# Kernel optimization log

Measured on AMD Instinct MI355X. Metric: run time of the kernel, lower is better.

The kernel has to match this reference:

```python
import jax, jax.numpy as jnp
import numpy as np

EPS = 1e-06


def setup_inputs() -> dict:
    key = jax.random.key(0)
    ks = jax.random.split(key, 8)
    B, N, D, r, T, O, Hid = 32, 2048, 64, 32, 31, 12, 128
    in_dim = r + T  # 63
    xav = lambda k, shape: jax.random.uniform(k, shape, jnp.float32, -1.0, 1.0) * np.sqrt(6.0 / (shape[0] + shape[1]))
    return {
        "H": jax.random.normal(ks[0], (B, N, D), jnp.float32),
        "ts_out": jax.random.uniform(ks[1], (B, O, T), jnp.float32),
        "O": O,
        "P_raw": xav(ks[2], (N, r)),
        "Q_raw": xav(ks[3], (N, r)),
        "W1": xav(ks[4], (in_dim, Hid)),
        "b1": jnp.zeros((Hid,), jnp.float32),
        "W2": xav(ks[5], (Hid, r)),
        "b2": jnp.zeros((r,), jnp.float32),
        "alpha": jax.random.uniform(ks[6], (1,), jnp.float32),
    }


def reference(H, ts_out, O, P_raw, Q_raw, W1, b1, W2, b2, alpha):
    # nonnegative_basis=True -> softplus on both bases
    P = jax.nn.softplus(P_raw)  # [N, r]
    Q = jax.nn.softplus(Q_raw)  # [N, r]
    # Right contraction: U = Q^T H per batch -> [B, r, D]
    U = jnp.einsum('bnd,nr->brd', H, Q)
    # Context norm over feature dim: [B, r]
    ctx = jnp.sqrt(jnp.mean(U * U, axis=-1) + EPS)
    # Gate features: concat([ts_out [B,O,T], ctx broadcast to [B,O,r]])
    B = H.shape[0]
    ctx_exp = jnp.broadcast_to(ctx[:, None, :], (B, O, ctx.shape[-1]))
    feat = jnp.concatenate([ts_out, ctx_exp], axis=-1)  # [B, O, T+r]
    # scale MLP with exact (erf) GELU, dropout=0 (eval)
    h = jax.nn.gelu(feat @ W1 + b1, approximate=False)
    s = jax.nn.softplus(h @ W2 + b2)  # [B, O, r]
    # M = P (s \odot U) without materializing NxN: [B, O, N, D]
    M = jnp.einsum('bor,brd,nr->bond', s, U, P)
    a = jnp.clip(alpha[0], 0.0, 1.0)
    H_base = H[:, None, :, :]  # broadcast over O
    H_graph = H_base + a * (M - H_base)
    return H_graph
```

## Files before the change

### kernel.cpp

```cpp
#include <hip/hip_runtime.h>
#include <math.h>

#define B_ 32
#define N_ 2048
#define D_ 64
#define R_ 32
#define T_ 31
#define O_ 12
#define HID_ 128
#define IN_DIM_ 63
#define NCH_ 32

#define OFF_QSP   0
#define OFF_UPART (OFF_QSP + N_*R_)
#define OFF_U     (OFF_UPART + B_*NCH_*R_*D_)
#define OFF_CTX   (OFF_U + B_*R_*D_)
#define OFF_PBF   (OFF_CTX + B_*R_)
#define OFF_SUT   (OFF_PBF + N_*R_/2)

typedef __attribute__((ext_vector_type(4))) float f32x4;
typedef __attribute__((ext_vector_type(8))) short short8;

__device__ __forceinline__ float softplus_f(float x) {
    return fmaxf(x, 0.0f) + log1pf(expf(-fabsf(x)));
}
__device__ __forceinline__ float gelu_f(float x) {
    return 0.5f * x * (1.0f + erff(x * 0.70710678118654752440f));
}
__device__ __forceinline__ unsigned short f2bf(float f) {
    unsigned int u = __float_as_uint(f);
    u = (u + 0x7FFFu + ((u >> 16) & 1u)) >> 16;
    return (unsigned short)u;
}

__global__ __launch_bounds__(256) void k_softplus(const float* __restrict__ Qr,
                                                  const float* __restrict__ Pr,
                                                  float* __restrict__ ws) {
    int i = blockIdx.x * blockDim.x + threadIdx.x;
    if (i < N_ * R_) {
        ws[OFF_QSP + i] = softplus_f(Qr[i]);
    } else if (i < 2 * N_ * R_) {
        int j = i - N_ * R_;
        ((unsigned short*)(ws + OFF_PBF))[j] = f2bf(softplus_f(Pr[j]));
    }
}

__global__ __launch_bounds__(512) void k_upart(const float* __restrict__ H,
                                               float* __restrict__ ws) {
    const float* __restrict__ Qsp = ws + OFF_QSP;
    float* __restrict__ Upart = ws + OFF_UPART;
    int b = blockIdx.x / NCH_;
    int c = blockIdx.x % NCH_;
    int tid = threadIdx.x;
    int d = tid & 63;
    int rb = __builtin_amdgcn_readfirstlane(tid >> 6);
    const int r0 = rb * 4;
    float acc0 = 0.f, acc1 = 0.f, acc2 = 0.f, acc3 = 0.f;
    const int n0 = c * (N_ / NCH_);
    const float* __restrict__ Hb = H + (size_t)b * N_ * D_ + d;
    #pragma unroll 2
    for (int i = 0; i < N_ / NCH_; ++i) {
        int n = n0 + i;
        float h = Hb[(size_t)n * D_];
        const float* q = Qsp + (size_t)n * R_ + r0;
        acc0 = fmaf(h, q[0], acc0);
        acc1 = fmaf(h, q[1], acc1);
        acc2 = fmaf(h, q[2], acc2);
        acc3 = fmaf(h, q[3], acc3);
    }
    float* up = Upart + ((size_t)(b * NCH_ + c) * R_ + r0) * D_ + d;
    up[0 * D_] = acc0;
    up[1 * D_] = acc1;
    up[2 * D_] = acc2;
    up[3 * D_] = acc3;
}

__global__ __launch_bounds__(256) void k_ured(float* __restrict__ ws) {
    const float* __restrict__ Upart = ws + OFF_UPART;
    float* __restrict__ U = ws + OFF_U;
    float* __restrict__ ctx = ws + OFF_CTX;
    int b = blockIdx.x;
    int r = blockIdx.y * 4 + (threadIdx.x >> 6);
    int d = threadIdx.x & 63;
    float u = 0.f;
    #pragma unroll 8
    for (int c = 0; c < NCH_; ++c)
        u += Upart[((size_t)(b * NCH_ + c) * R_ + r) * D_ + d];
    U[((size_t)b * R_ + r) * D_ + d] = u;
    float sq = u * u;
    #pragma unroll
    for (int off = 32; off; off >>= 1) sq += __shfl_xor(sq, off, 64);
    if (d == 0) ctx[b * R_ + r] = sqrtf(sq * (1.0f / D_) + 1e-6f);
}

__global__ __launch_bounds__(128) void k_mlp(const float* __restrict__ ts_out,
                                             const float* __restrict__ W1,
                                             const float* __restrict__ b1,
                                             const float* __restrict__ W2,
                                             const float* __restrict__ b2,
                                             const float* __restrict__ alpha,
                                             float* __restrict__ ws) {
    __shared__ float feat[IN_DIM_];
    __shared__ float hsh[HID_];
    __shared__ float ssh[R_];
    int bo = blockIdx.x;
    int b = bo / O_;
    int tid = threadIdx.x;
    const float* __restrict__ ctx = ws + OFF_CTX;
    if (tid < T_) feat[tid] = ts_out[(size_t)bo * T_ + tid];
    else if (tid < IN_DIM_) feat[tid] = ctx[b * R_ + (tid - T_)];
    __syncthreads();
    float acc = b1[tid];
    #pragma unroll 9
    for (int k = 0; k < IN_DIM_; ++k) acc = fmaf(feat[k], W1[k * HID_ + tid], acc);
    hsh[tid] = gelu_f(acc);
    __syncthreads();
    if (tid < R_) {
        float a2 = b2[tid];
        #pragma unroll 8
        for (int j = 0; j < HID_; ++j) a2 = fmaf(hsh[j], W2[j * R_ + tid], a2);
        ssh[tid] = softplus_f(a2);
    }
    __syncthreads();
    float a = fminf(fmaxf(alpha[0], 0.0f), 1.0f);
    const float* __restrict__ U = ws + OFF_U;
    unsigned short* SUT = (unsigned short*)(ws + OFF_SUT) + (size_t)bo * D_ * R_;
    #pragma unroll
    for (int idx = tid; idx < D_ * R_; idx += 128) {
        int d = idx >> 5, r = idx & 31;
        SUT[idx] = f2bf(a * ssh[r] * U[((size_t)b * R_ + r) * D_ + d]);
    }
}

__global__ __launch_bounds__(256) void k_main(const float* __restrict__ H,
                                              const float* __restrict__ alpha,
                                              const float* __restrict__ ws,
                                              float* __restrict__ out) {
    __shared__ float tile[64 * 64];
    const int b = blockIdx.y;
    const int nblk = blockIdx.x * 64;
    const int tid = threadIdx.x;
    const int w = tid >> 6;
    const int lane = tid & 63;
    const int l16 = lane & 15;
    const int lhi = lane >> 4;
    const int rl = w * 16 + l16;
    const float a = fminf(fmaxf(alpha[0], 0.0f), 1.0f);
    const float oma = 1.0f - a;

    const unsigned short* Pbf = (const unsigned short*)(ws + OFF_PBF);
    const unsigned short* SUT0 = (const unsigned short*)(ws + OFF_SUT);

    short8 pfrag = *(const short8*)(Pbf + (size_t)(nblk + rl) * R_ + lhi * 8);

    const float* __restrict__ Hrow = H + ((size_t)b * N_ + nblk + rl) * D_;
    f32x4 homa[4];
    #pragma unroll
    for (int db = 0; db < 4; ++db)
        homa[db] = oma * *(const f32x4*)(Hrow + db * 16 + lhi * 4);

    char* tbytes = (char*)tile;
    float* __restrict__ oblk = out + ((size_t)(b * O_) * N_ + nblk) * D_;

    for (int o = 0; o < O_; ++o) {
        const unsigned short* SUT = SUT0 + (size_t)(b * O_ + o) * D_ * R_;
        #pragma unroll
        for (int db = 0; db < 4; ++db) {
            short8 sfrag = *(const short8*)(SUT + (size_t)(db * 16 + l16) * R_ + lhi * 8);
            f32x4 v = homa[db] + __builtin_amdgcn_mfma_f32_16x16x32_bf16(
                sfrag, pfrag, (f32x4){0.f, 0.f, 0.f, 0.f}, 0, 0, 0);
            int c = (db * 64 + lhi * 16) ^ ((rl & 7) << 4);
            *(f32x4*)(tbytes + rl * 256 + c) = v;
        }
        __syncthreads();
        char* op = (char*)(oblk + (size_t)o * N_ * D_);
        #pragma unroll
        for (int i = 0; i < 4; ++i) {
            int g = i * 4096 + tid * 16;
            int rr = g >> 8;
            int cc = (g & 255) ^ ((rr & 7) << 4);
            f32x4 v = *(const f32x4*)(tbytes + rr * 256 + cc);
            *(f32x4*)(op + g) = v;
        }
        __syncthreads();
    }
}

extern "C" void kernel_launch(void* const* d_in, const int* in_sizes, int n_in,
                              void* d_out, int out_size, void* d_ws, size_t ws_size,
                              hipStream_t stream) {
    const float* H      = (const float*)d_in[0];
    const float* ts_out = (const float*)d_in[1];
    const float* P_raw  = (const float*)d_in[3];
    const float* Q_raw  = (const float*)d_in[4];
    const float* W1     = (const float*)d_in[5];
    const float* b1     = (const float*)d_in[6];
    const float* W2     = (const float*)d_in[7];
    const float* b2     = (const float*)d_in[8];
    const float* alpha  = (const float*)d_in[9];
    float* out = (float*)d_out;
    float* ws  = (float*)d_ws;

    k_softplus<<<dim3((2 * N_ * R_ + 255) / 256), dim3(256), 0, stream>>>(Q_raw, P_raw, ws);
    k_upart<<<dim3(B_ * NCH_), dim3(512), 0, stream>>>(H, ws);
    k_ured<<<dim3(B_, 8), dim3(256), 0, stream>>>(ws);
    k_mlp<<<dim3(B_ * O_), dim3(128), 0, stream>>>(ts_out, W1, b1, W2, b2, alpha, ws);
    k_main<<<dim3(N_ / 64, B_), dim3(256), 0, stream>>>(H, alpha, ws, out);
}
```

Measured before the change: 73.52 us.

## Remove block barriers in main kernel via wave-private LDS rows and double buffering

Changes the output staging so each wave reads back only the LDS rows it wrote itself. This makes both __syncthreads per output slice unnecessary, so they are dropped. The loop also handles two O slices per iteration, loading both S fragments up front and using two LDS buffers. The aim is to cut barrier stalls and overlap fragment loads in a store-bound kernel, at the cost of twice the LDS per block, which may lower occupancy.

```diff
diff --git a/kernel.cpp b/kernel.cpp
--- a/kernel.cpp
+++ b/kernel.cpp
@@ -136,7 +136,7 @@
                                               const float* __restrict__ alpha,
                                               const float* __restrict__ ws,
                                               float* __restrict__ out) {
-    __shared__ float tile[64 * 64];
+    __shared__ float tile[2 * 64 * 64];
     const int b = blockIdx.y;
     const int nblk = blockIdx.x * 64;
     const int tid = threadIdx.x;
@@ -159,30 +159,43 @@
     for (int db = 0; db < 4; ++db)
         homa[db] = oma * *(const f32x4*)(Hrow + db * 16 + lhi * 4);
 
-    char* tbytes = (char*)tile;
+    char* t0 = (char*)tile;
+    char* t1 = (char*)tile + 16384;
     float* __restrict__ oblk = out + ((size_t)(b * O_) * N_ + nblk) * D_;
 
-    for (int o = 0; o < O_; ++o) {
-        const unsigned short* SUT = SUT0 + (size_t)(b * O_ + o) * D_ * R_;
+    for (int o = 0; o < O_; o += 2) {
+        const unsigned short* S0 = SUT0 + (size_t)(b * O_ + o) * D_ * R_;
+        const unsigned short* S1 = S0 + D_ * R_;
+        short8 sf[8];
         #pragma unroll
         for (int db = 0; db < 4; ++db) {
-            short8 sfrag = *(const short8*)(SUT + (size_t)(db * 16 + l16) * R_ + lhi * 8);
-            f32x4 v = homa[db] + __builtin_amdgcn_mfma_f32_16x16x32_bf16(
-                sfrag, pfrag, (f32x4){0.f, 0.f, 0.f, 0.f}, 0, 0, 0);
-            int c = (db * 64 + lhi * 16) ^ ((rl & 7) << 4);
-            *(f32x4*)(tbytes + rl * 256 + c) = v;
+            sf[db]     = *(const short8*)(S0 + (size_t)(db * 16 + l16) * R_ + lhi * 8);
+            sf[4 + db] = *(const short8*)(S1 + (size_t)(db * 16 + l16) * R_ + lhi * 8);
         }
-        __syncthreads();
-        char* op = (char*)(oblk + (size_t)o * N_ * D_);
         #pragma unroll
-        for (int i = 0; i < 4; ++i) {
-            int g = i * 4096 + tid * 16;
-            int rr = g >> 8;
-            int cc = (g & 255) ^ ((rr & 7) << 4);
-            f32x4 v = *(const f32x4*)(tbytes + rr * 256 + cc);
-            *(f32x4*)(op + g) = v;
+        for (int h = 0; h < 2; ++h) {
+            char* tb = h ? t1 : t0;
+            #pragma unroll
+            for (int db = 0; db < 4; ++db) {
+                f32x4 v = homa[db] + __builtin_amdgcn_mfma_f32_16x16x32_bf16(
+                    sf[h * 4 + db], pfrag, (f32x4){0.f, 0.f, 0.f, 0.f}, 0, 0, 0);
+                int c = (db * 64 + lhi * 16) ^ ((rl & 7) << 4);
+                *(f32x4*)(tb + rl * 256 + c) = v;
+            }
         }
-        __syncthreads();
+        #pragma unroll
+        for (int h = 0; h < 2; ++h) {
+            char* tb = h ? t1 : t0;
+            char* op = (char*)(oblk + (size_t)(o + h) * N_ * D_);
+            #pragma unroll
+            for (int i = 0; i < 4; ++i) {
+                int g = w * 4096 + i * 1024 + lane * 16;
+                int rr = g >> 8;
+                int cc = (g & 255) ^ ((rr & 7) << 4);
+                f32x4 v = *(const f32x4*)(tb + rr * 256 + cc);
+                *(f32x4*)(op + g) = v;
+            }
+        }
     }
 }
 
```

After: 73.68 us. Within noise of the previous version (+0.2%).
